# Kernel tuning notes

Hardware: AMD Instinct MI355X
Metric: run time of the kernel (lower is better)

Reference implementation:

```python
import jax, jax.numpy as jnp
import numpy as np

COMMITMENT_COST = 0.25
CODEBOOK_SIZE = 1024
EMBED_DIM = 256


def setup_inputs() -> dict:
    key = jax.random.key(0)
    k1, k2 = jax.random.split(key)
    inputs = jax.random.normal(k1, (128, 512, EMBED_DIM), dtype=jnp.float32)
    embedding = jax.random.normal(k2, (CODEBOOK_SIZE, EMBED_DIM), dtype=jnp.float32)
    return {"inputs": inputs, "embedding": embedding}


def reference(inputs, embedding):
    input_shape = inputs.shape
    K, D = embedding.shape
    flat = inputs.reshape(-1, D)  # [N, D]

    distances = (
        jnp.sum(flat * flat, axis=1, keepdims=True)
        + jnp.sum(embedding * embedding, axis=1)
        - 2.0 * jnp.matmul(flat, embedding.T)
    )
    encoding_indices = jnp.argmin(distances, axis=1)  # [N]

    # one-hot scatter (torch scatter_ of ones) then matmul lookup
    encodings = jax.nn.one_hot(encoding_indices, K, dtype=flat.dtype)  # [N, K]
    quantized = jnp.matmul(encodings, embedding).reshape(input_shape)

    e_latent_loss = jnp.mean(jnp.square(jax.lax.stop_gradient(quantized) - inputs))
    vq_loss = COMMITMENT_COST * e_latent_loss

    # straight-through estimator
    quantized_st = inputs + jax.lax.stop_gradient(quantized - inputs)

    avg_probs = jnp.mean(encodings, axis=0)  # [K]
    perplexity = jnp.exp(-jnp.sum(avg_probs * jnp.log(avg_probs + 1e-10)))
    return vq_loss, quantized_st, perplexity, encodings
```

## Files before the change

### kernel.cpp

```cpp
#include <hip/hip_runtime.h>
#include <hip/hip_bf16.h>


constexpr int NTOK = 65536;
constexpr int D    = 256;
constexpr int K    = 1024;

typedef __attribute__((ext_vector_type(8))) short short8v;
typedef __attribute__((ext_vector_type(4))) float f32x4;

#define MFMA_B16(a, b, c) __builtin_amdgcn_mfma_f32_16x16x32_bf16(a, b, c, 0, 0, 0)

static __device__ __forceinline__ void bf16split(float f, short& h, short& l) {
  __hip_bfloat16 bh = __float2bfloat16(f);
  float fh = __bfloat162float(bh);
  __hip_bfloat16 bl = __float2bfloat16(f - fh);
  h = __builtin_bit_cast(short, bh);
  l = __builtin_bit_cast(short, bl);
}

__global__ __launch_bounds__(256) void prep_kernel(
    const float* __restrict__ emb, short* __restrict__ ehf,
    short* __restrict__ elf, float* __restrict__ e2n) {
  const int c    = (int)blockIdx.x * 256 + (int)threadIdx.x;
  const int tile = c >> 4, cc = c & 15;
  const float* er = emb + (size_t)c * 256;
  float s = 0.f;
  #pragma unroll
  for (int ks = 0; ks < 8; ++ks) {
    #pragma unroll
    for (int g = 0; g < 4; ++g) {
      short8v hv, lv;
      #pragma unroll
      for (int j = 0; j < 8; ++j) {
        float f = er[ks * 32 + g * 8 + j];
        s = fmaf(f, f, s);
        short h, l;
        bf16split(f, h, l);
        hv[j] = h;
        lv[j] = l;
      }
      const size_t off = ((size_t)(tile * 8 + ks) * 64 + g * 16 + cc) * 8;
      *reinterpret_cast<short8v*>(ehf + off) = hv;
      *reinterpret_cast<short8v*>(elf + off) = lv;
    }
  }
  e2n[c] = s;
}

__global__ __launch_bounds__(256, 2) void argmin_kernel(
    const float* __restrict__ x, const short* __restrict__ ehf,
    const short* __restrict__ elf, const float* __restrict__ e2n,
    int* __restrict__ out_idx, int* __restrict__ fixup_cnt,
    int* __restrict__ fixup_list) {
  const int lane = (int)threadIdx.x & 63;
  const int wid  = (int)blockIdx.x * 4 + ((int)threadIdx.x >> 6);
  const int tok0 = wid * 32;
  const int row  = lane & 15;
  const int kgrp = lane >> 4;

  short8v xh0[8], xl0[8], xh1[8], xl1[8];
  {
    const float* xr0 = x + (size_t)(tok0 + row) * 256 + kgrp * 8;
    const float* xr1 = xr0 + 16 * 256;
    #pragma unroll
    for (int ks = 0; ks < 8; ++ks) {
      float4 u0 = *reinterpret_cast<const float4*>(xr0 + ks * 32);
      float4 u1 = *reinterpret_cast<const float4*>(xr0 + ks * 32 + 4);
      float4 v0 = *reinterpret_cast<const float4*>(xr1 + ks * 32);
      float4 v1 = *reinterpret_cast<const float4*>(xr1 + ks * 32 + 4);
      const float uf[8] = {u0.x, u0.y, u0.z, u0.w, u1.x, u1.y, u1.z, u1.w};
      const float vf[8] = {v0.x, v0.y, v0.z, v0.w, v1.x, v1.y, v1.z, v1.w};
      #pragma unroll
      for (int j = 0; j < 8; ++j) {
        short h, l;
        bf16split(uf[j], h, l);
        xh0[ks][j] = h; xl0[ks][j] = l;
        bf16split(vf[j], h, l);
        xh1[ks][j] = h; xl1[ks][j] = l;
      }
    }
  }

  float best[8], second[8];
  int   bidx[8];
  #pragma unroll
  for (int s = 0; s < 8; ++s) { best[s] = 3.4e38f; second[s] = 3.4e38f; bidx[s] = 0; }

  const short8v* ehv = reinterpret_cast<const short8v*>(ehf);
  const short8v* elv = reinterpret_cast<const short8v*>(elf);

  for (int tile = 0; tile < 64; ++tile) {
    f32x4 a0 = {0.f, 0.f, 0.f, 0.f}, a1 = a0, a2 = a0;
    f32x4 b0 = a0, b1 = a0, b2 = a0;
    const short8v* ep = ehv + (size_t)tile * 512 + lane;
    const short8v* lp = elv + (size_t)tile * 512 + lane;
    #pragma unroll
    for (int ks = 0; ks < 8; ++ks) {
      short8v eh = ep[ks * 64];
      short8v el = lp[ks * 64];
      a0 = MFMA_B16(xh0[ks], eh, a0);
      b0 = MFMA_B16(xh1[ks], eh, b0);
      a1 = MFMA_B16(xl0[ks], eh, a1);
      b1 = MFMA_B16(xl1[ks], eh, b1);
      a2 = MFMA_B16(xh0[ks], el, a2);
      b2 = MFMA_B16(xh1[ks], el, b2);
    }
    const int   code = tile * 16 + (lane & 15);
    const float e2v  = e2n[code];
    #pragma unroll
    for (int i = 0; i < 4; ++i) {
      {
        const float d = fmaf(-2.f, (a0[i] + a1[i]) + a2[i], e2v);
        if (d < best[i]) { second[i] = best[i]; best[i] = d; bidx[i] = code; }
        else if (d < second[i]) second[i] = d;
      }
      {
        const float d = fmaf(-2.f, (b0[i] + b1[i]) + b2[i], e2v);
        if (d < best[4 + i]) { second[4 + i] = best[4 + i]; best[4 + i] = d; bidx[4 + i] = code; }
        else if (d < second[4 + i]) second[4 + i] = d;
      }
    }
  }

  #pragma unroll
  for (int m = 1; m < 16; m <<= 1) {
    #pragma unroll
    for (int s = 0; s < 8; ++s) {
      const float ob = __shfl_xor(best[s], m);
      const float os = __shfl_xor(second[s], m);
      const int   oi = __shfl_xor(bidx[s], m);
      const float nsec = fminf(fmaxf(best[s], ob), fminf(second[s], os));
      if (ob < best[s] || (ob == best[s] && oi < bidx[s])) {
        best[s] = ob;
        bidx[s] = oi;
      }
      second[s] = nsec;
    }
  }
  if ((lane & 15) == 0) {
    #pragma unroll
    for (int s = 0; s < 8; ++s) {
      const int token = tok0 + (s >> 2) * 16 + kgrp * 4 + (s & 3);
      out_idx[token] = bidx[s];
      if (second[s] - best[s] < 0.25f) {
        int p = atomicAdd(fixup_cnt, 1);
        if (p < NTOK) fixup_list[p] = token;
      }
    }
  }
}

__global__ __launch_bounds__(256) void fixup_kernel(
    const float* __restrict__ x, const float* __restrict__ emb,
    const float* __restrict__ e2n, const int* __restrict__ fixup_cnt,
    const int* __restrict__ fixup_list, int* __restrict__ out_idx) {
  const int lane   = (int)threadIdx.x & 63;
  const int gw     = (int)blockIdx.x * 4 + ((int)threadIdx.x >> 6);
  const int nwaves = (int)gridDim.x * 4;
  int n = *fixup_cnt;
  if (n > NTOK) n = NTOK;
  for (int fi = gw; fi < n; fi += nwaves) {
    const int token = fixup_list[fi];
    if ((unsigned)token >= (unsigned)NTOK) continue;
    const float4* xr = reinterpret_cast<const float4*>(x + (size_t)token * 256);
    float bv = 3.4e38f;
    int   bi = 0;
    for (int ci = 0; ci < 16; ++ci) {
      const int c = ci * 64 + lane;
      const float4* er = reinterpret_cast<const float4*>(emb + (size_t)c * 256);
      float s0 = 0.f, s1 = 0.f, s2 = 0.f, s3 = 0.f;
      #pragma unroll 8
      for (int q = 0; q < 64; ++q) {
        float4 xv = xr[q], ev = er[q];
        s0 = fmaf(xv.x, ev.x, s0);
        s1 = fmaf(xv.y, ev.y, s1);
        s2 = fmaf(xv.z, ev.z, s2);
        s3 = fmaf(xv.w, ev.w, s3);
      }
      const float dist = fmaf(-2.f, (s0 + s1) + (s2 + s3), e2n[c]);
      if (dist < bv) { bv = dist; bi = c; }
    }
    #pragma unroll
    for (int m = 1; m < 64; m <<= 1) {
      const float ob = __shfl_xor(bv, m);
      const int   oi = __shfl_xor(bi, m);
      if (ob < bv || (ob == bv && oi < bi)) { bv = ob; bi = oi; }
    }
    if (lane == 0) out_idx[token] = bi;
  }
}

__global__ __launch_bounds__(256) void output_kernel(
    const float* __restrict__ x, const float* __restrict__ emb,
    const int* __restrict__ idx, float* __restrict__ qout,
    float* __restrict__ enc, int* __restrict__ hist,
    double* __restrict__ lossacc) {
  const int lane = threadIdx.x & 63;
  const int gw   = (int)((blockIdx.x * 256 + threadIdx.x) >> 6);
  float lsum = 0.f;
  for (int tok = gw; tok < NTOK; tok += 32768) {
    const int ki = idx[tok];
    float4 xv = reinterpret_cast<const float4*>(x + (size_t)tok * D)[lane];
    float4 ev = reinterpret_cast<const float4*>(emb + (size_t)ki * D)[lane];
    float dx = ev.x - xv.x, dy = ev.y - xv.y, dz = ev.z - xv.z,
          dw = ev.w - xv.w;
    float4 q;
    q.x = xv.x + dx; q.y = xv.y + dy; q.z = xv.z + dz; q.w = xv.w + dw;
    reinterpret_cast<float4*>(qout + (size_t)tok * D)[lane] = q;
    lsum += dx * dx + dy * dy + dz * dz + dw * dw;
    float4* erow = reinterpret_cast<float4*>(enc + (size_t)tok * K);
    #pragma unroll
    for (int r = 0; r < 4; ++r) {
      const int fi = r * 64 + lane;
      float4 z;
      z.x = (fi * 4 + 0 == ki) ? 1.f : 0.f;
      z.y = (fi * 4 + 1 == ki) ? 1.f : 0.f;
      z.z = (fi * 4 + 2 == ki) ? 1.f : 0.f;
      z.w = (fi * 4 + 3 == ki) ? 1.f : 0.f;
      erow[fi] = z;
    }
    if (lane == 0) atomicAdd(&hist[ki], 1);
  }
  #pragma unroll
  for (int m = 1; m < 64; m <<= 1) lsum += __shfl_xor(lsum, m);
  __shared__ float wsum[4];
  if (lane == 0) wsum[threadIdx.x >> 6] = lsum;
  __syncthreads();
  if (threadIdx.x == 0) {
    double tt = (double)wsum[0] + (double)wsum[1] + (double)wsum[2] +
                (double)wsum[3];
    atomicAdd(lossacc, tt);
  }
}

__global__ __launch_bounds__(256) void finalize_kernel(
    const int* __restrict__ hist, const double* __restrict__ lossacc,
    float* __restrict__ out_loss, float* __restrict__ out_perp) {
  const int lane = threadIdx.x & 63;
  float part = 0.f;
  for (int k = threadIdx.x; k < K; k += 256) {
    float p = (float)hist[k] * (1.0f / 65536.0f);
    part += p * logf(p + 1e-10f);
  }
  #pragma unroll
  for (int m = 1; m < 64; m <<= 1) part += __shfl_xor(part, m);
  __shared__ float wsum[4];
  if (lane == 0) wsum[threadIdx.x >> 6] = part;
  __syncthreads();
  if (threadIdx.x == 0) {
    float ent = wsum[0] + wsum[1] + wsum[2] + wsum[3];
    out_loss[0] = 0.25f * (float)(lossacc[0] * (1.0 / 16777216.0));
    out_perp[0] = expf(-ent);
  }
}

extern "C" void kernel_launch(void* const* d_in, const int* in_sizes, int n_in,
                              void* d_out, int out_size, void* d_ws,
                              size_t ws_size, hipStream_t stream) {
  const float* x   = (const float*)d_in[0];
  const float* emb = (const float*)d_in[1];
  float* out       = (float*)d_out;

  float* loss_out = out;
  float* q_out    = out + 1;
  float* perp_out = out + 1 + (size_t)NTOK * D;
  float* enc_out  = perp_out + 1;

  char*   wsb  = (char*)d_ws;
  int*    idx  = (int*)wsb;
  float*  e2n  = (float*)(wsb + 262144);
  int*    hist = (int*)(wsb + 266240);
  double* acc  = (double*)(wsb + 270336);
  int*    fcnt = (int*)(wsb + 270344);

  short* ehf;
  short* elf;
  int*   flist;
  if (ws_size >= (size_t)270400 + 524288 * 2 + 262144) {
    ehf   = (short*)(wsb + 270400);
    elf   = (short*)(wsb + 270400 + 524288);
    flist = (int*)(wsb + 270400 + 1048576);
  } else {
    ehf   = (short*)(enc_out + (size_t)67108864 - 262144);
    elf   = (short*)(enc_out + (size_t)67108864 - 131072);
    flist = (int*)(q_out + (size_t)16777216 - 65536);
  }

  hipMemsetAsync(wsb + 266240, 0, 8192, stream);

  prep_kernel<<<4, 256, 0, stream>>>(emb, ehf, elf, e2n);
  argmin_kernel<<<512, 256, 0, stream>>>(x, ehf, elf, e2n, idx, fcnt, flist);
  fixup_kernel<<<512, 256, 0, stream>>>(x, emb, e2n, fcnt, flist, idx);
  output_kernel<<<8192, 256, 0, stream>>>(x, emb, idx, q_out, enc_out, hist,
                                          acc);
  finalize_kernel<<<1, 256, 0, stream>>>(hist, acc, loss_out, perp_out);
}
```

Measured before the change: 924.7 us.

## Replace shuffle-based argmin reduction with LDS scatter and per-token serial reduction

Instead of assuming a fixed MFMA output layout and reducing best/second/index across 16 lanes with xor shuffles, each lane's output slot (token row, code column) is recovered by running probe MFMAs on constant inputs. The per-lane partial results are scattered into shared memory and then reduced serially by 128 threads, one token each. This removes 4 rounds of 24 shuffles per wave and makes the layout mapping robust. In exchange it adds shared memory, two block barriers, a per-i e2n load inside the tile loop, and widens the fixup margin from 0.25 to 0.5, which may enlarge the fixup list.

```diff
diff --git a/kernel.cpp b/kernel.cpp
--- a/kernel.cpp
+++ b/kernel.cpp
@@ -53,15 +53,47 @@
     const short* __restrict__ elf, const float* __restrict__ e2n,
     int* __restrict__ out_idx, int* __restrict__ fixup_cnt,
     int* __restrict__ fixup_list) {
-  const int lane = (int)threadIdx.x & 63;
-  const int wid  = (int)blockIdx.x * 4 + ((int)threadIdx.x >> 6);
-  const int tok0 = wid * 32;
-  const int row  = lane & 15;
-  const int kgrp = lane >> 4;
+  __shared__ float Mb[4][2][16][16];
+  __shared__ float Ms[4][2][16][16];
+  __shared__ int   Mi[4][2][16][16];
+  const int tid  = (int)threadIdx.x;
+  const int lane = tid & 63;
+  const int wib  = tid >> 6;
+  const int tok0 = ((int)blockIdx.x * 4 + wib) * 32;
+
+  {
+    float* pb = &Mb[0][0][0][0];
+    float* ps = &Ms[0][0][0][0];
+    int*   pi = &Mi[0][0][0][0];
+    #pragma unroll
+    for (int u = 0; u < 8; ++u) {
+      pb[tid * 8 + u] = 3.4e38f;
+      ps[tid * 8 + u] = 3.4e38f;
+      pi[tid * 8 + u] = 0x7fffffff;
+    }
+  }
+
+  int t_slot[4], c_slot[4];
+  {
+    const short one_s = __builtin_bit_cast(short, __float2bfloat16(1.0f));
+    const short row_s =
+        __builtin_bit_cast(short, __float2bfloat16((float)(lane & 15)));
+    short8v ones, rowv;
+    #pragma unroll
+    for (int j = 0; j < 8; ++j) { ones[j] = one_s; rowv[j] = row_s; }
+    f32x4 zz = {0.f, 0.f, 0.f, 0.f};
+    f32x4 prow = MFMA_B16(rowv, ones, zz);
+    f32x4 pcol = MFMA_B16(ones, rowv, zz);
+    #pragma unroll
+    for (int i = 0; i < 4; ++i) {
+      t_slot[i] = ((int)(prow[i] * 0.03125f + 0.5f)) & 15;
+      c_slot[i] = ((int)(pcol[i] * 0.03125f + 0.5f)) & 15;
+    }
+  }
 
   short8v xh0[8], xl0[8], xh1[8], xl1[8];
   {
-    const float* xr0 = x + (size_t)(tok0 + row) * 256 + kgrp * 8;
+    const float* xr0 = x + (size_t)(tok0 + (lane & 15)) * 256 + (lane >> 4) * 8;
     const float* xr1 = xr0 + 16 * 256;
     #pragma unroll
     for (int ks = 0; ks < 8; ++ks) {
@@ -106,10 +138,10 @@
       a2 = MFMA_B16(xh0[ks], el, a2);
       b2 = MFMA_B16(xh1[ks], el, b2);
     }
-    const int   code = tile * 16 + (lane & 15);
-    const float e2v  = e2n[code];
     #pragma unroll
     for (int i = 0; i < 4; ++i) {
+      const int   code = tile * 16 + c_slot[i];
+      const float e2v  = e2n[code];
       {
         const float d = fmaf(-2.f, (a0[i] + a1[i]) + a2[i], e2v);
         if (d < best[i]) { second[i] = best[i]; best[i] = d; bidx[i] = code; }
@@ -123,30 +155,37 @@
     }
   }
 
-  #pragma unroll
-  for (int m = 1; m < 16; m <<= 1) {
-    #pragma unroll
-    for (int s = 0; s < 8; ++s) {
-      const float ob = __shfl_xor(best[s], m);
-      const float os = __shfl_xor(second[s], m);
-      const int   oi = __shfl_xor(bidx[s], m);
-      const float nsec = fminf(fmaxf(best[s], ob), fminf(second[s], os));
-      if (ob < best[s] || (ob == best[s] && oi < bidx[s])) {
-        best[s] = ob;
-        bidx[s] = oi;
-      }
-      second[s] = nsec;
-    }
-  }
-  if ((lane & 15) == 0) {
-    #pragma unroll
-    for (int s = 0; s < 8; ++s) {
-      const int token = tok0 + (s >> 2) * 16 + kgrp * 4 + (s & 3);
-      out_idx[token] = bidx[s];
-      if (second[s] - best[s] < 0.25f) {
-        int p = atomicAdd(fixup_cnt, 1);
-        if (p < NTOK) fixup_list[p] = token;
-      }
+  __syncthreads();
+  #pragma unroll
+  for (int half = 0; half < 2; ++half) {
+    #pragma unroll
+    for (int i = 0; i < 4; ++i) {
+      const int s = half * 4 + i;
+      Mb[wib][half][t_slot[i]][c_slot[i]] = best[s];
+      Ms[wib][half][t_slot[i]][c_slot[i]] = second[s];
+      Mi[wib][half][t_slot[i]][c_slot[i]] = bidx[s];
+    }
+  }
+  __syncthreads();
+  if (tid < 128) {
+    const int w = tid >> 5, h = (tid >> 4) & 1, t = tid & 15;
+    float b  = Mb[w][h][t][0];
+    float s2 = Ms[w][h][t][0];
+    int   id = Mi[w][h][t][0];
+    #pragma unroll
+    for (int c = 1; c < 16; ++c) {
+      const float ob = Mb[w][h][t][c];
+      const float os = Ms[w][h][t][c];
+      const int   oi = Mi[w][h][t][c];
+      const float ns = fminf(fmaxf(b, ob), fminf(s2, os));
+      if (ob < b || (ob == b && oi < id)) { b = ob; id = oi; }
+      s2 = ns;
+    }
+    const int token = (int)blockIdx.x * 128 + w * 32 + h * 16 + t;
+    out_idx[token] = id;
+    if (s2 - b < 0.5f) {
+      int p = atomicAdd(fixup_cnt, 1);
+      if (p < NTOK) fixup_list[p] = token;
     }
   }
 }
```

After: 1.048 ms. 13.4% more time.
